# Performance work log

Hardware: AMD Instinct MI355X
Metric: run time of the kernel (lower is better)

## Reference

```python
import jax, jax.numpy as jnp
import numpy as np

HIDDEN = 2048
QK_DIM = 2048
NUM_HEADS = 16
HEAD_DIM = QK_DIM // NUM_HEADS  # 128; RoPE rotates this many dims per head
B, T = 4, 2048
EPS = 1e-5


def setup_inputs() -> dict:
    key = jax.random.key(0)
    ks = jax.random.split(key, 10)
    return {
        "q_state": jax.random.normal(ks[0], (B, T, HIDDEN), jnp.float32),
        "k_state": jax.random.normal(ks[1], (B, T, HIDDEN), jnp.float32),
        "v_state": jax.random.normal(ks[2], (B, T, HIDDEN), jnp.float32),
        # torch Linear weights: [out_features, in_features], no bias
        "Wq": jax.random.normal(ks[3], (QK_DIM, HIDDEN), jnp.float32) * 0.02,
        "Wk": jax.random.normal(ks[4], (QK_DIM, HIDDEN), jnp.float32) * 0.02,
        "Wv": jax.random.normal(ks[5], (HIDDEN, HIDDEN), jnp.float32) * 0.02,
        "negator": jnp.asarray(1.0, jnp.float32),
        "q_gamma": jnp.ones((2 * QK_DIM,), jnp.float32),
        "q_beta": jnp.zeros((2 * QK_DIM,), jnp.float32),
        "k_gamma": jnp.ones((2 * QK_DIM,), jnp.float32),
        "k_beta": jnp.zeros((2 * QK_DIM,), jnp.float32),
        "offset": 0,
    }


def _layer_norm(x, gamma, beta):
    mu = jnp.mean(x, axis=-1, keepdims=True)
    var = jnp.mean(jnp.square(x - mu), axis=-1, keepdims=True)
    return (x - mu) * jax.lax.rsqrt(var + EPS) * gamma + beta


def _split_heads(x, n_heads):
    b, t, d = x.shape
    return x.reshape(b, t, n_heads, d // n_heads).transpose(0, 2, 1, 3)  # b h t f


def _rotate_half(x):
    # interleaved pairs: (x1, x2) -> (-x2, x1)
    x2 = x.reshape(*x.shape[:-1], x.shape[-1] // 2, 2)
    return jnp.stack((-x2[..., 1], x2[..., 0]), axis=-1).reshape(x.shape)


def _apply_rope(x, offset, rot_dim):
    # x: [b, h, t, f]; rotate first rot_dim features, pass the rest through
    t = (jnp.arange(x.shape[-2]) + offset).astype(jnp.float32)
    inv_freq = 1.0 / (10000.0 ** (jnp.arange(0, rot_dim, 2, dtype=jnp.float32) / rot_dim))
    freqs = t[:, None] * inv_freq[None, :]           # [t, rot_dim/2]
    freqs = jnp.repeat(freqs, 2, axis=-1)            # [t, rot_dim] interleaved
    cos, sin = jnp.cos(freqs), jnp.sin(freqs)
    xl, xr = x[..., :rot_dim], x[..., rot_dim:]
    xl = xl * cos + _rotate_half(xl) * sin
    return jnp.concatenate([xl, xr], axis=-1)


def reference(q_state, k_state, v_state, Wq, Wk, Wv, negator,
              q_gamma, q_beta, k_gamma, k_beta, offset):
    q = jnp.einsum("btd,fd->btf", q_state, Wq)
    k = jnp.einsum("btd,fd->btf", k_state, Wk)
    v = jnp.einsum("btd,fd->btf", v_state, Wv)
    q = jnp.concatenate((q, negator - q), axis=-1)   # [b, t, 2*QK_DIM]
    k = jnp.concatenate((k, negator - k), axis=-1)
    q = _layer_norm(q, q_gamma, q_beta)
    k = _layer_norm(k, k_gamma, k_beta)
    q = _split_heads(q, NUM_HEADS)                   # [b, h, t, 2*HEAD_DIM]
    k = _split_heads(k, NUM_HEADS)
    v = _split_heads(v, NUM_HEADS)                   # [b, h, t, HIDDEN/h]
    q = _apply_rope(q, offset, HEAD_DIM)
    k = _apply_rope(k, offset, HEAD_DIM)
    return q, k, v
```

## Files before the change

### kernel.cpp

```cpp
#include <hip/hip_runtime.h>
#include <hip/hip_fp16.h>

#define TDIM 2048
#define BDIM 4
#define MROWS 8192
#define NDIM 2048
#define KDIM 2048
#define NH 16

typedef __attribute__((ext_vector_type(8))) _Float16 f16x8;
typedef __attribute__((ext_vector_type(4))) _Float16 f16x4;
typedef __attribute__((ext_vector_type(4))) float f32x4;

__device__ __forceinline__ void load16_to_lds(const _Float16* g, _Float16* l) {
  __builtin_amdgcn_global_load_lds((const __attribute__((address_space(1))) void*)g,
                                   (__attribute__((address_space(3))) void*)l,
                                   16, 0, 0);
}

#define WAITBAR(N) do { \
  asm volatile("s_waitcnt vmcnt(" #N ")" ::: "memory"); \
  __builtin_amdgcn_s_barrier(); \
  __builtin_amdgcn_sched_barrier(0); \
} while (0)

#define LGKM0_FENCE() do { \
  asm volatile("s_waitcnt lgkmcnt(0)" ::: "memory"); \
  __builtin_amdgcn_sched_barrier(0); \
} while (0)

__global__ __launch_bounds__(256) void cvt7_kernel(
    const float* __restrict__ s0, const float* __restrict__ s1,
    const float* __restrict__ s2, const float* __restrict__ s3,
    const float* __restrict__ s4, const float* __restrict__ s5,
    _Float16* __restrict__ d0, _Float16* __restrict__ d1,
    _Float16* __restrict__ d2, _Float16* __restrict__ d3,
    _Float16* __restrict__ d4, _Float16* __restrict__ d5,
    const int* __restrict__ offset_p, float* __restrict__ rope_tab) {
  const int z = blockIdx.z;
  if (z == 6) {
    const int idx = blockIdx.x * blockDim.x + threadIdx.x;
    if (idx < TDIM * 64) {
      const int t = idx >> 6, p = idx & 63;
      const float tpos = (float)(t + offset_p[0]);
      const float invf = exp2f(-(float)p * 0.20762050592854797f);
      float sv, cv;
      sincosf(tpos * invf, &sv, &cv);
      rope_tab[idx * 2 + 0] = cv;
      rope_tab[idx * 2 + 1] = sv;
    }
    return;
  }
  const float* s; _Float16* d; int n;
  switch (z) {
    case 0: s = s0; d = d0; n = MROWS * KDIM; break;
    case 1: s = s1; d = d1; n = MROWS * KDIM; break;
    case 2: s = s2; d = d2; n = MROWS * KDIM; break;
    case 3: s = s3; d = d3; n = NDIM * KDIM; break;
    case 4: s = s4; d = d4; n = NDIM * KDIM; break;
    default: s = s5; d = d5; n = NDIM * KDIM; break;
  }
  const int n8 = n >> 3;
  const int stride = gridDim.x * blockDim.x;
  for (int i = blockIdx.x * blockDim.x + threadIdx.x; i < n8; i += stride) {
    float4 f0 = ((const float4*)s)[i * 2 + 0];
    float4 f1 = ((const float4*)s)[i * 2 + 1];
    f16x8 h;
    h[0] = (_Float16)f0.x; h[1] = (_Float16)f0.y;
    h[2] = (_Float16)f0.z; h[3] = (_Float16)f0.w;
    h[4] = (_Float16)f1.x; h[5] = (_Float16)f1.y;
    h[6] = (_Float16)f1.z; h[7] = (_Float16)f1.w;
    ((f16x8*)d)[i] = h;
  }
}

__global__ __launch_bounds__(512, 2) void gemm_kernel(
    const _Float16* __restrict__ A0, const _Float16* __restrict__ A1,
    const _Float16* __restrict__ A2,
    const _Float16* __restrict__ W0, const _Float16* __restrict__ W1,
    const _Float16* __restrict__ W2,
    _Float16* __restrict__ qraw, _Float16* __restrict__ kraw,
    float* __restrict__ vout) {
  __shared__ __align__(16) _Float16 lds[4][2][8192];

  int lin = (blockIdx.z * gridDim.y + blockIdx.y) * gridDim.x + blockIdx.x;
  lin = (lin & 7) * 96 + (lin >> 3);
  const int z  = lin >> 8;
  const int ty = (lin >> 3) & 31;
  const int tx = lin & 7;

  const _Float16* __restrict__ A  = (z == 0) ? A0 : ((z == 1) ? A1 : A2);
  const _Float16* __restrict__ Wt = (z == 0) ? W0 : ((z == 1) ? W1 : W2);
  const int m0 = ty * 256;
  const int n0 = tx * 256;

  const int tid  = threadIdx.x;
  const int wave = tid >> 6;
  const int lane = tid & 63;
  const int m_in = lane & 15;
  const int kq   = lane >> 4;
  const int wave_m = wave >> 2;
  const int wave_n = wave & 3;

  f32x4 acc[8][4];
  const f32x4 z4 = {0.f, 0.f, 0.f, 0.f};
#pragma unroll
  for (int i = 0; i < 8; ++i)
#pragma unroll
    for (int j = 0; j < 4; ++j) acc[i][j] = z4;

  const int P0 = tid * 16;
  const int P1 = (512 + tid) * 16;
  const int L0 = P0 ^ (((P0 >> 7) & 3) << 4);
  const int L1 = P1 ^ (((P1 >> 7) & 3) << 4);
  const _Float16* srcA0 = A  + (size_t)(m0 + (L0 >> 6)) * KDIM + ((L0 & 63) >> 1);
  const _Float16* srcA1 = A  + (size_t)(m0 + (L1 >> 6)) * KDIM + ((L1 & 63) >> 1);
  const _Float16* srcB0 = Wt + (size_t)(n0 + (L0 >> 6)) * KDIM + ((L0 & 63) >> 1);
  const _Float16* srcB1 = Wt + (size_t)(n0 + (L1 >> 6)) * KDIM + ((L1 & 63) >> 1);
  const int dst0 = (wave * 64) * 8;
  const int dst1 = (512 + wave * 64) * 8;

  int offA[8], offB[4];
#pragma unroll
  for (int mi = 0; mi < 8; ++mi) {
    const int r = wave_m * 128 + mi * 16 + m_in;
    offA[mi] = r * 64 + ((kq ^ ((r >> 1) & 3)) << 4);
  }
#pragma unroll
  for (int ni = 0; ni < 4; ++ni) {
    const int r = wave_n * 64 + ni * 16 + m_in;
    offB[ni] = r * 64 + ((kq ^ ((r >> 1) & 3)) << 4);
  }

  auto stageA = [&](int kt) {
    _Float16* base = &lds[kt & 3][0][0];
    const int ko = kt * 32;
    load16_to_lds(srcA0 + ko, base + dst0);
    load16_to_lds(srcA1 + ko, base + dst1);
  };
  auto stageB = [&](int kt) {
    _Float16* base = &lds[kt & 3][0][0];
    const int ko = kt * 32;
    load16_to_lds(srcB0 + ko, base + 8192 + dst0);
    load16_to_lds(srcB1 + ko, base + 8192 + dst1);
  };

  f16x8 a[8], b[4];

  auto kstep_p1 = [&](int kt, int stage_kt) {
    const char* Ab = (const char*)&lds[kt & 3][0][0];
    const char* Bb = (const char*)&lds[kt & 3][1][0];
#pragma unroll
    for (int mi = 0; mi < 8; ++mi) a[mi] = *(const f16x8*)(Ab + offA[mi]);
    b[0] = *(const f16x8*)(Bb + offB[0]);
    b[1] = *(const f16x8*)(Bb + offB[1]);
    if (stage_kt >= 0) stageA(stage_kt);
    LGKM0_FENCE();
    __builtin_amdgcn_s_setprio(1);
#pragma unroll
    for (int mi = 0; mi < 8; ++mi)
#pragma unroll
      for (int ni = 0; ni < 2; ++ni)
        acc[mi][ni] = __builtin_amdgcn_mfma_f32_16x16x32_f16(a[mi], b[ni], acc[mi][ni], 0, 0, 0);
    __builtin_amdgcn_s_setprio(0);
    __builtin_amdgcn_s_barrier();
    __builtin_amdgcn_sched_barrier(0);
  };
  auto kstep_p2 = [&](int kt, int stage_kt) {
    const char* Bb = (const char*)&lds[kt & 3][1][0];
    b[2] = *(const f16x8*)(Bb + offB[2]);
    b[3] = *(const f16x8*)(Bb + offB[3]);
    if (stage_kt >= 0) stageB(stage_kt);
    LGKM0_FENCE();
    __builtin_amdgcn_s_setprio(1);
#pragma unroll
    for (int mi = 0; mi < 8; ++mi)
#pragma unroll
      for (int ni = 2; ni < 4; ++ni)
        acc[mi][ni] = __builtin_amdgcn_mfma_f32_16x16x32_f16(a[mi], b[ni], acc[mi][ni], 0, 0, 0);
    __builtin_amdgcn_s_setprio(0);
  };

  stageA(0); stageB(0); stageA(1); stageB(1); stageA(2); stageB(2);
  WAITBAR(8);

#pragma unroll 1
  for (int kt = 0; kt < KDIM / 32 - 3; ++kt) {
    kstep_p1(kt, kt + 3);
    kstep_p2(kt, kt + 3);
    WAITBAR(8);
  }
  kstep_p1(KDIM / 32 - 3, -1); kstep_p2(KDIM / 32 - 3, -1); WAITBAR(4);
  kstep_p1(KDIM / 32 - 2, -1); kstep_p2(KDIM / 32 - 2, -1); WAITBAR(0);
  kstep_p1(KDIM / 32 - 1, -1); kstep_p2(KDIM / 32 - 1, -1);

  const int rbase = kq * 4;
  const int wm = wave_m * 128;
  const int wn = wave_n * 64;
  if (z < 2) {
    _Float16* __restrict__ raw = (z == 0) ? qraw : kraw;
    _Float16* cst = &lds[0][0][0];
    __syncthreads();
#pragma unroll
    for (int mi = 0; mi < 8; ++mi) {
      const int row = wm + mi * 16 + rbase;
#pragma unroll
      for (int ni = 0; ni < 4; ++ni) {
        const int col = wn + ni * 16 + m_in;
#pragma unroll
        for (int r = 0; r < 4; ++r)
          cst[(row + r) * 256 + col] = (_Float16)acc[mi][ni][r];
      }
    }
    __syncthreads();
#pragma unroll
    for (int j = 0; j < 16; ++j) {
      const int c = j * 512 + tid;
      const int row = c >> 5, col8 = (c & 31) * 8;
      *(f16x8*)&raw[(size_t)(m0 + row) * NDIM + n0 + col8] =
          *(const f16x8*)&cst[row * 256 + col8];
    }
  } else {
#pragma unroll
    for (int mi = 0; mi < 8; ++mi) {
      const int mb = m0 + wm + mi * 16 + rbase;
#pragma unroll
      for (int ni = 0; ni < 4; ++ni) {
        const int n = n0 + wn + ni * 16 + m_in;
        const int h = n >> 7, dd = n & 127;
#pragma unroll
        for (int r = 0; r < 4; ++r) {
          const int m = mb + r;
          const int b = m >> 11, t = m & 2047;
          vout[(((size_t)(b * NH + h) * TDIM) + t) * 128 + dd] = acc[mi][ni][r];
        }
      }
    }
  }
}

__global__ __launch_bounds__(256) void ln_rope_kernel(
    const _Float16* __restrict__ qraw, const _Float16* __restrict__ kraw,
    const float* __restrict__ negator,
    const float* __restrict__ q_gamma, const float* __restrict__ q_beta,
    const float* __restrict__ k_gamma, const float* __restrict__ k_beta,
    const float* __restrict__ rope_tab,
    float* __restrict__ out) {
  const int row = blockIdx.x;
  const int mat = blockIdx.y;
  const _Float16* __restrict__ raw = mat ? kraw : qraw;
  const float* __restrict__ gamma = mat ? k_gamma : q_gamma;
  const float* __restrict__ beta  = mat ? k_beta  : q_beta;
  float* __restrict__ outb = out + (size_t)mat * ((size_t)BDIM * NH * TDIM * 256);

  const float c = negator[0];
  const float mu = 0.5f * c;
  const int tid = threadIdx.x;

  __shared__ __align__(16) float vals[2048];
  __shared__ float wred[4];

  const int b = row >> 11, t = row & 2047;

  f16x8 hv = ((const f16x8*)(raw + (size_t)row * 2048))[tid];
  float v[8];
  float ss = 0.f;
#pragma unroll
  for (int j = 0; j < 8; ++j) {
    float x = (float)hv[j] - mu;
    v[j] = x;
    ss += x * x;
  }
  ((float4*)vals)[tid * 2 + 0] = make_float4(v[0], v[1], v[2], v[3]);
  ((float4*)vals)[tid * 2 + 1] = make_float4(v[4], v[5], v[6], v[7]);

#pragma unroll
  for (int o = 32; o > 0; o >>= 1) ss += __shfl_down(ss, o, 64);
  if ((tid & 63) == 0) wred[tid >> 6] = ss;
  __syncthreads();
  const float var = (wred[0] + wred[1] + wred[2] + wred[3]) * (1.0f / 2048.0f);
  const float rstd = rsqrtf(var + 1e-5f);

  const float4* __restrict__ tab4 = (const float4*)(rope_tab + (size_t)t * 128);

#pragma unroll
  for (int j = 0; j < 4; ++j) {
    const int g0 = j * 1024 + tid * 4;
    const float sgn = (g0 < 2048) ? 1.f : -1.f;
    const float4 val = ((const float4*)vals)[(g0 & 2047) >> 2];
    const float4 gm  = ((const float4*)gamma)[g0 >> 2];
    const float4 bt  = ((const float4*)beta)[g0 >> 2];
    float y0 = sgn * val.x * rstd * gm.x + bt.x;
    float y1 = sgn * val.y * rstd * gm.y + bt.y;
    float y2 = sgn * val.z * rstd * gm.z + bt.z;
    float y3 = sgn * val.w * rstd * gm.w + bt.w;

    const int h  = g0 >> 8;
    const int d0 = g0 & 255;
    float4 res;
    if (d0 < 128) {
      const float4 cs = tab4[d0 >> 2];
      res.x = y0 * cs.x - y1 * cs.y;
      res.y = y1 * cs.x + y0 * cs.y;
      res.z = y2 * cs.z - y3 * cs.w;
      res.w = y3 * cs.z + y2 * cs.w;
    } else {
      res = make_float4(y0, y1, y2, y3);
    }
    ((float4*)(outb + (((size_t)(b * NH + h) * TDIM) + t) * 256))[d0 >> 2] = res;
  }
}

extern "C" void kernel_launch(void* const* d_in, const int* in_sizes, int n_in,
                              void* d_out, int out_size, void* d_ws, size_t ws_size,
                              hipStream_t stream) {
  (void)in_sizes; (void)n_in; (void)out_size; (void)ws_size;
  const float* q_state = (const float*)d_in[0];
  const float* k_state = (const float*)d_in[1];
  const float* v_state = (const float*)d_in[2];
  const float* Wq = (const float*)d_in[3];
  const float* Wk = (const float*)d_in[4];
  const float* Wv = (const float*)d_in[5];
  const float* negator = (const float*)d_in[6];
  const float* q_gamma = (const float*)d_in[7];
  const float* q_beta  = (const float*)d_in[8];
  const float* k_gamma = (const float*)d_in[9];
  const float* k_beta  = (const float*)d_in[10];
  const int* offset    = (const int*)d_in[11];

  float* out = (float*)d_out;
  float* vout = out + (size_t)2 * BDIM * NH * TDIM * 256;

  _Float16* Aq   = (_Float16*)d_ws;
  _Float16* Ak   = Aq + (size_t)MROWS * KDIM;
  _Float16* Av   = Ak + (size_t)MROWS * KDIM;
  _Float16* Wq16 = Av + (size_t)MROWS * KDIM;
  _Float16* Wk16 = Wq16 + (size_t)NDIM * KDIM;
  _Float16* Wv16 = Wk16 + (size_t)NDIM * KDIM;
  _Float16* qraw = Wv16 + (size_t)NDIM * KDIM;
  _Float16* kraw = qraw + (size_t)MROWS * NDIM;
  float* rope_tab = (float*)(kraw + (size_t)MROWS * NDIM);

  cvt7_kernel<<<dim3(2048, 1, 7), dim3(256), 0, stream>>>(
      q_state, k_state, v_state, Wq, Wk, Wv, Aq, Ak, Av, Wq16, Wk16, Wv16,
      offset, rope_tab);

  gemm_kernel<<<dim3(8, 32, 3), dim3(512), 0, stream>>>(
      Aq, Ak, Av, Wq16, Wk16, Wv16, qraw, kraw, vout);

  ln_rope_kernel<<<dim3(8192, 2), dim3(256), 0, stream>>>(
      qraw, kraw, negator, q_gamma, q_beta, k_gamma, k_beta, rope_tab, out);
}
```

Measured before the change: 735.4 us.

## Double-buffer GEMM register fragments to overlap LDS reads with MFMA

The GEMM main loop now uses a ping-pong software pipeline. While the MFMAs for step kt run on one set of register fragments, the A/B fragments for step kt+1 are read from LDS into a second set. The global-to-LDS staging of A and B is merged into a single stage call per k-step, and the loop takes one barrier per k-step instead of two split half-steps. This aims to hide LDS read latency and cut synchronisation, at the cost of about 48 extra VGPRs per thread for the second fragment set, which could hurt occupancy or cause spills.

```diff
diff --git a/kernel.cpp b/kernel.cpp
--- a/kernel.cpp
+++ b/kernel.cpp
@@ -18,7 +18,7 @@
                                    16, 0, 0);
 }
 
-#define WAITBAR(N) do { \
+#define VB_BAR(N) do { \
   asm volatile("s_waitcnt vmcnt(" #N ")" ::: "memory"); \
   __builtin_amdgcn_s_barrier(); \
   __builtin_amdgcn_sched_barrier(0); \
@@ -28,6 +28,8 @@
   asm volatile("s_waitcnt lgkmcnt(0)" ::: "memory"); \
   __builtin_amdgcn_sched_barrier(0); \
 } while (0)
+
+#define SCHED_FENCE() __builtin_amdgcn_sched_barrier(0)
 
 __global__ __launch_bounds__(256) void cvt7_kernel(
     const float* __restrict__ s0, const float* __restrict__ s1,
@@ -132,67 +134,76 @@
     offB[ni] = r * 64 + ((kq ^ ((r >> 1) & 3)) << 4);
   }
 
-  auto stageA = [&](int kt) {
+  auto stage = [&](int kt) {
     _Float16* base = &lds[kt & 3][0][0];
     const int ko = kt * 32;
     load16_to_lds(srcA0 + ko, base + dst0);
     load16_to_lds(srcA1 + ko, base + dst1);
-  };
-  auto stageB = [&](int kt) {
-    _Float16* base = &lds[kt & 3][0][0];
-    const int ko = kt * 32;
     load16_to_lds(srcB0 + ko, base + 8192 + dst0);
     load16_to_lds(srcB1 + ko, base + 8192 + dst1);
   };
 
-  f16x8 a[8], b[4];
-
-  auto kstep_p1 = [&](int kt, int stage_kt) {
+  f16x8 aA[8], bA[4], aB[8], bB[4];
+
+  auto readfr = [&](f16x8 (&a)[8], f16x8 (&b)[4], int kt) {
     const char* Ab = (const char*)&lds[kt & 3][0][0];
     const char* Bb = (const char*)&lds[kt & 3][1][0];
 #pragma unroll
     for (int mi = 0; mi < 8; ++mi) a[mi] = *(const f16x8*)(Ab + offA[mi]);
-    b[0] = *(const f16x8*)(Bb + offB[0]);
-    b[1] = *(const f16x8*)(Bb + offB[1]);
-    if (stage_kt >= 0) stageA(stage_kt);
-    LGKM0_FENCE();
+#pragma unroll
+    for (int ni = 0; ni < 4; ++ni) b[ni] = *(const f16x8*)(Bb + offB[ni]);
+  };
+  auto domfma = [&](f16x8 (&a)[8], f16x8 (&b)[4]) {
     __builtin_amdgcn_s_setprio(1);
 #pragma unroll
     for (int mi = 0; mi < 8; ++mi)
 #pragma unroll
-      for (int ni = 0; ni < 2; ++ni)
-        acc[mi][ni] = __builtin_amdgcn_mfma_f32_16x16x32_f16(a[mi], b[ni], acc[mi][ni], 0, 0, 0);
-    __builtin_amdgcn_s_setprio(0);
-    __builtin_amdgcn_s_barrier();
-    __builtin_amdgcn_sched_barrier(0);
-  };
-  auto kstep_p2 = [&](int kt, int stage_kt) {
-    const char* Bb = (const char*)&lds[kt & 3][1][0];
-    b[2] = *(const f16x8*)(Bb + offB[2]);
-    b[3] = *(const f16x8*)(Bb + offB[3]);
-    if (stage_kt >= 0) stageB(stage_kt);
-    LGKM0_FENCE();
-    __builtin_amdgcn_s_setprio(1);
-#pragma unroll
-    for (int mi = 0; mi < 8; ++mi)
-#pragma unroll
-      for (int ni = 2; ni < 4; ++ni)
+      for (int ni = 0; ni < 4; ++ni)
         acc[mi][ni] = __builtin_amdgcn_mfma_f32_16x16x32_f16(a[mi], b[ni], acc[mi][ni], 0, 0, 0);
     __builtin_amdgcn_s_setprio(0);
   };
 
-  stageA(0); stageB(0); stageA(1); stageB(1); stageA(2); stageB(2);
-  WAITBAR(8);
+  stage(0); stage(1); stage(2);
+  VB_BAR(8);
+  readfr(aA, bA, 0);
+  LGKM0_FENCE();
 
 #pragma unroll 1
-  for (int kt = 0; kt < KDIM / 32 - 3; ++kt) {
-    kstep_p1(kt, kt + 3);
-    kstep_p2(kt, kt + 3);
-    WAITBAR(8);
-  }
-  kstep_p1(KDIM / 32 - 3, -1); kstep_p2(KDIM / 32 - 3, -1); WAITBAR(4);
-  kstep_p1(KDIM / 32 - 2, -1); kstep_p2(KDIM / 32 - 2, -1); WAITBAR(0);
-  kstep_p1(KDIM / 32 - 1, -1); kstep_p2(KDIM / 32 - 1, -1);
+  for (int kt = 0; kt < 60; kt += 2) {
+    stage(kt + 3);
+    VB_BAR(8);
+    readfr(aB, bB, kt + 1);
+    SCHED_FENCE();
+    domfma(aA, bA);
+    LGKM0_FENCE();
+
+    stage(kt + 4);
+    VB_BAR(8);
+    readfr(aA, bA, kt + 2);
+    SCHED_FENCE();
+    domfma(aB, bB);
+    LGKM0_FENCE();
+  }
+  stage(63);
+  VB_BAR(8);
+  readfr(aB, bB, 61);
+  SCHED_FENCE();
+  domfma(aA, bA);
+  LGKM0_FENCE();
+
+  VB_BAR(4);
+  readfr(aA, bA, 62);
+  SCHED_FENCE();
+  domfma(aB, bB);
+  LGKM0_FENCE();
+
+  VB_BAR(0);
+  readfr(aB, bB, 63);
+  SCHED_FENCE();
+  domfma(aA, bA);
+  LGKM0_FENCE();
+
+  domfma(aB, bB);
 
   const int rbase = kq * 4;
   const int wm = wave_m * 128;
```

Result: slower. 761.2 us (+3.5%).

## Restructure GEMM k-loop into four interleaved phases with finer LDS reads

Applied to the files above, without the earlier changes.

Splits each k-step of the fp16 MFMA GEMM main loop into four phases. Each phase reads half of the A fragments or half of the B fragments from LDS, issues one global-to-LDS stage load, hits a barrier, then runs 8 MFMAs, replacing the earlier two phases of 16 MFMAs. This lowers register pressure (a[4] instead of a[8]) and spreads LDS reads and global stage loads more evenly between MFMA bursts. The cost is more barriers per k-step, which can add synchronisation stalls.

```diff
diff --git a/kernel.cpp b/kernel.cpp
--- a/kernel.cpp
+++ b/kernel.cpp
@@ -18,15 +18,20 @@
                                    16, 0, 0);
 }
 
-#define WAITBAR(N) do { \
+#define SCHED_FENCE() __builtin_amdgcn_sched_barrier(0)
+
+#define PHASE_BAR() do { \
+  SCHED_FENCE(); \
+  __builtin_amdgcn_s_barrier(); \
+  asm volatile("s_waitcnt lgkmcnt(0)" ::: "memory"); \
+  SCHED_FENCE(); \
+} while (0)
+
+#define VB_BAR(N) do { \
+  SCHED_FENCE(); \
   asm volatile("s_waitcnt vmcnt(" #N ")" ::: "memory"); \
   __builtin_amdgcn_s_barrier(); \
-  __builtin_amdgcn_sched_barrier(0); \
-} while (0)
-
-#define LGKM0_FENCE() do { \
-  asm volatile("s_waitcnt lgkmcnt(0)" ::: "memory"); \
-  __builtin_amdgcn_sched_barrier(0); \
+  SCHED_FENCE(); \
 } while (0)
 
 __global__ __launch_bounds__(256) void cvt7_kernel(
@@ -132,67 +137,72 @@
     offB[ni] = r * 64 + ((kq ^ ((r >> 1) & 3)) << 4);
   }
 
-  auto stageA = [&](int kt) {
-    _Float16* base = &lds[kt & 3][0][0];
-    const int ko = kt * 32;
-    load16_to_lds(srcA0 + ko, base + dst0);
-    load16_to_lds(srcA1 + ko, base + dst1);
+  auto stage_q0 = [&](int kt) { load16_to_lds(srcA0 + kt * 32, &lds[kt & 3][0][0] + dst0); };
+  auto stage_q1 = [&](int kt) { load16_to_lds(srcA1 + kt * 32, &lds[kt & 3][0][0] + dst1); };
+  auto stage_q2 = [&](int kt) { load16_to_lds(srcB0 + kt * 32, &lds[kt & 3][0][0] + 8192 + dst0); };
+  auto stage_q3 = [&](int kt) { load16_to_lds(srcB1 + kt * 32, &lds[kt & 3][0][0] + 8192 + dst1); };
+
+  f16x8 a[4], b01[2], b23[2];
+
+  auto rdA = [&](int kt, int half) {
+    const char* Ab = (const char*)&lds[kt & 3][0][0];
+#pragma unroll
+    for (int mi = 0; mi < 4; ++mi) a[mi] = *(const f16x8*)(Ab + offA[half * 4 + mi]);
   };
-  auto stageB = [&](int kt) {
-    _Float16* base = &lds[kt & 3][0][0];
-    const int ko = kt * 32;
-    load16_to_lds(srcB0 + ko, base + 8192 + dst0);
-    load16_to_lds(srcB1 + ko, base + 8192 + dst1);
+  auto rdB01 = [&](int kt) {
+    const char* Bb = (const char*)&lds[kt & 3][1][0];
+    b01[0] = *(const f16x8*)(Bb + offB[0]);
+    b01[1] = *(const f16x8*)(Bb + offB[1]);
   };
-
-  f16x8 a[8], b[4];
-
-  auto kstep_p1 = [&](int kt, int stage_kt) {
-    const char* Ab = (const char*)&lds[kt & 3][0][0];
+  auto rdB23 = [&](int kt) {
     const char* Bb = (const char*)&lds[kt & 3][1][0];
-#pragma unroll
-    for (int mi = 0; mi < 8; ++mi) a[mi] = *(const f16x8*)(Ab + offA[mi]);
-    b[0] = *(const f16x8*)(Bb + offB[0]);
-    b[1] = *(const f16x8*)(Bb + offB[1]);
-    if (stage_kt >= 0) stageA(stage_kt);
-    LGKM0_FENCE();
+    b23[0] = *(const f16x8*)(Bb + offB[2]);
+    b23[1] = *(const f16x8*)(Bb + offB[3]);
+  };
+  auto mf8 = [&](int mbase, f16x8 (&bb)[2], int nbase) {
     __builtin_amdgcn_s_setprio(1);
 #pragma unroll
-    for (int mi = 0; mi < 8; ++mi)
+    for (int mi = 0; mi < 4; ++mi)
 #pragma unroll
       for (int ni = 0; ni < 2; ++ni)
-        acc[mi][ni] = __builtin_amdgcn_mfma_f32_16x16x32_f16(a[mi], b[ni], acc[mi][ni], 0, 0, 0);
-    __builtin_amdgcn_s_setprio(0);
-    __builtin_amdgcn_s_barrier();
-    __builtin_amdgcn_sched_barrier(0);
-  };
-  auto kstep_p2 = [&](int kt, int stage_kt) {
-    const char* Bb = (const char*)&lds[kt & 3][1][0];
-    b[2] = *(const f16x8*)(Bb + offB[2]);
-    b[3] = *(const f16x8*)(Bb + offB[3]);
-    if (stage_kt >= 0) stageB(stage_kt);
-    LGKM0_FENCE();
-    __builtin_amdgcn_s_setprio(1);
-#pragma unroll
-    for (int mi = 0; mi < 8; ++mi)
-#pragma unroll
-      for (int ni = 2; ni < 4; ++ni)
-        acc[mi][ni] = __builtin_amdgcn_mfma_f32_16x16x32_f16(a[mi], b[ni], acc[mi][ni], 0, 0, 0);
+        acc[mbase + mi][nbase + ni] =
+            __builtin_amdgcn_mfma_f32_16x16x32_f16(a[mi], bb[ni], acc[mbase + mi][nbase + ni], 0, 0, 0);
     __builtin_amdgcn_s_setprio(0);
   };
 
-  stageA(0); stageB(0); stageA(1); stageB(1); stageA(2); stageB(2);
-  WAITBAR(8);
+  stage_q0(0); stage_q1(0); stage_q2(0); stage_q3(0);
+  stage_q0(1); stage_q1(1); stage_q2(1); stage_q3(1);
+  stage_q0(2); stage_q1(2); stage_q2(2); stage_q3(2);
+  VB_BAR(8);
 
 #pragma unroll 1
-  for (int kt = 0; kt < KDIM / 32 - 3; ++kt) {
-    kstep_p1(kt, kt + 3);
-    kstep_p2(kt, kt + 3);
-    WAITBAR(8);
-  }
-  kstep_p1(KDIM / 32 - 3, -1); kstep_p2(KDIM / 32 - 3, -1); WAITBAR(4);
-  kstep_p1(KDIM / 32 - 2, -1); kstep_p2(KDIM / 32 - 2, -1); WAITBAR(0);
-  kstep_p1(KDIM / 32 - 1, -1); kstep_p2(KDIM / 32 - 1, -1);
+  for (int j = 0; j <= 60; ++j) {
+    const int s = j + 3;
+    rdA(j, 0); rdB01(j); stage_q0(s);
+    PHASE_BAR();
+    mf8(0, b01, 0);
+    rdB23(j); stage_q1(s);
+    PHASE_BAR();
+    mf8(0, b23, 2);
+    rdA(j, 1); stage_q2(s);
+    PHASE_BAR();
+    mf8(4, b23, 2);
+    stage_q3(s);
+    VB_BAR(8);
+    mf8(4, b01, 0);
+  }
+  rdA(61, 0); rdB01(61); PHASE_BAR(); mf8(0, b01, 0);
+  rdB23(61);             PHASE_BAR(); mf8(0, b23, 2);
+  rdA(61, 1);            PHASE_BAR(); mf8(4, b23, 2);
+  VB_BAR(4);             mf8(4, b01, 0);
+  rdA(62, 0); rdB01(62); PHASE_BAR(); mf8(0, b01, 0);
+  rdB23(62);             PHASE_BAR(); mf8(0, b23, 2);
+  rdA(62, 1);            PHASE_BAR(); mf8(4, b23, 2);
+  VB_BAR(0);             mf8(4, b01, 0);
+  rdA(63, 0); rdB01(63); PHASE_BAR(); mf8(0, b01, 0);
+  rdB23(63);             PHASE_BAR(); mf8(0, b23, 2);
+  rdA(63, 1);            PHASE_BAR(); mf8(4, b23, 2);
+  mf8(4, b01, 0);
 
   const int rbase = kq * 4;
   const int wm = wave_m * 128;
```

New measurement: 735.9 us. Within noise of the previous version (+0.1%).
